# Optimization experiments

Hardware: AMD Instinct MI355X
Metric: run time of the kernel (lower is better)

Reference implementation:

```python
import jax, jax.numpy as jnp
import numpy as np

IN_CH = 128
OUT_CH = 128

def setup_inputs() -> dict:
    key = jax.random.key(0)
    k1, k2, k3, k4, k5 = jax.random.split(key, 5)
    from_tensor = jax.random.normal(k1, (640000, IN_CH), dtype=jnp.float32)
    to_index = jax.random.randint(k2, (640000,), 0, 10000, dtype=jnp.int64)
    # torch Linear default init ~ U(-1/sqrt(fan_in), 1/sqrt(fan_in))
    lim1 = 1.0 / np.sqrt(IN_CH)
    lim2 = 1.0 / np.sqrt(OUT_CH)
    W1 = jax.random.uniform(k3, (OUT_CH, IN_CH), jnp.float32, -lim1, lim1)
    b1 = jnp.zeros((OUT_CH,), jnp.float32)
    W2 = jax.random.uniform(k4, (OUT_CH, OUT_CH), jnp.float32, -lim2, lim2)
    b2 = jnp.zeros((OUT_CH,), jnp.float32)
    return {"from_tensor": from_tensor, "to_index": to_index, "dim_size": 10000,
            "W1": W1, "b1": b1, "W2": W2, "b2": b2}

def reference(from_tensor, to_index, dim_size, W1, b1, W2, b2):
    # MLP transform (transform_scatter=True): Linear+ReLU x2
    h = jax.nn.relu(from_tensor @ W1.T + b1)
    h = jax.nn.relu(h @ W2.T + b2)          # (num_src, OUT_CH)
    # scatter-mean over to_index into dim_size rows
    seg_sum = jax.ops.segment_sum(h, to_index, num_segments=dim_size)
    counts = jax.ops.segment_sum(jnp.ones((h.shape[0],), h.dtype), to_index,
                                 num_segments=dim_size)
    return seg_sum / jnp.maximum(counts, 1.0)[:, None]
```

## Files before the change

kernel.cpp:

```cpp
#include <hip/hip_runtime.h>
#include <hip/hip_bf16.h>

#define IN_CH 128
#define OUT_CH 128
#define LDSPAD 136

typedef short bf16x8 __attribute__((ext_vector_type(8)));
typedef float f32x4  __attribute__((ext_vector_type(4)));

__device__ __forceinline__ unsigned short f32_to_bf16_bits(float f) {
    unsigned u = __builtin_bit_cast(unsigned, f);
    u += 0x7FFFu + ((u >> 16) & 1u);
    return (unsigned short)(u >> 16);
}
__device__ __forceinline__ float bf16_bits_to_f32(unsigned short b) {
    return __builtin_bit_cast(float, (unsigned)b << 16);
}

__global__ void detect_kernel(const unsigned short* __restrict__ X,
                              const unsigned short* __restrict__ W1,
                              const unsigned short* __restrict__ W2,
                              const int* __restrict__ idx,
                              int* __restrict__ flags) {
    __shared__ int red[4];
    const int t = threadIdx.x;
    if (t < 4) red[t] = 0;
    __syncthreads();
    #pragma unroll
    for (int w = 0; w < 3; ++w) {
        const unsigned short* p = (w == 0) ? X : (w == 1) ? W1 : W2;
        int crazy = 0;
        for (int j = t; j < 512; j += 256) {
            const unsigned short h = p[j];
            const int e = (h >> 7) & 0xFF;
            const int man = h & 0x7F;
            if (e >= 0x90 || (e == 0 && man != 0)) crazy++;
        }
        if (crazy) atomicAdd(&red[w], crazy);
    }
    {
        if (idx[2 * t + 1] != 0) atomicAdd(&red[3], 1);
    }
    __syncthreads();
    if (t == 0) {
        flags[0] = red[0] > 16 ? 1 : 0;
        flags[1] = red[1] > 16 ? 1 : 0;
        flags[2] = red[2] > 16 ? 1 : 0;
        flags[3] = red[3] < 8  ? 1 : 0;
    }
}

__global__ void count_kernel(const int* __restrict__ idx, int* __restrict__ cnt,
                             const int* __restrict__ flags, int n) {
    const int sh = flags[3];
    int i = blockIdx.x * blockDim.x + threadIdx.x;
    if (i < n) atomicAdd(&cnt[idx[(size_t)i << sh]], 1);
}

__global__ __launch_bounds__(256)
void mlp_scatter_kernel(const unsigned short* __restrict__ X,
                        const int* __restrict__ idx,
                        const unsigned short* __restrict__ W1,
                        const unsigned short* __restrict__ B1,
                        const unsigned short* __restrict__ W2,
                        const unsigned short* __restrict__ B2,
                        float* __restrict__ seg_sum,
                        const int* __restrict__ flags,
                        int n_src, int n_tiles)
{
    __shared__ short lds_x[16 * LDSPAD];
    __shared__ short lds_h[16 * LDSPAD];

    const int xf32  = flags[0];
    const int w1f32 = flags[1];
    const int w2f32 = flags[2];
    const int i64   = flags[3];

    const int tid  = threadIdx.x;
    const int wave = tid >> 6;
    const int lane = tid & 63;
    const int m    = lane & 15;
    const int quad = lane >> 4;

    bf16x8 w1f[2][4], w2f[2][4];
    float  b1c[2], b2c[2];
    #pragma unroll
    for (int t = 0; t < 2; ++t) {
        const int n = wave * 32 + t * 16 + m;
        b1c[t] = w1f32 ? ((const float*)B1)[n] : bf16_bits_to_f32(B1[n]);
        b2c[t] = w2f32 ? ((const float*)B2)[n] : bf16_bits_to_f32(B2[n]);
        #pragma unroll
        for (int kc = 0; kc < 4; ++kc) {
            const int ko = kc * 32 + quad * 8;
            if (w1f32) {
                const float* Wf = (const float*)W1;
                f32x4 lo = *(const f32x4*)(Wf + n * IN_CH + ko);
                f32x4 hi = *(const f32x4*)(Wf + n * IN_CH + ko + 4);
                bf16x8 v;
                #pragma unroll
                for (int j = 0; j < 4; ++j) {
                    v[j]     = (short)f32_to_bf16_bits(lo[j]);
                    v[4 + j] = (short)f32_to_bf16_bits(hi[j]);
                }
                w1f[t][kc] = v;
            } else {
                w1f[t][kc] = *(const bf16x8*)(W1 + n * IN_CH + ko);
            }
            if (w2f32) {
                const float* Wf = (const float*)W2;
                f32x4 lo = *(const f32x4*)(Wf + n * OUT_CH + ko);
                f32x4 hi = *(const f32x4*)(Wf + n * OUT_CH + ko + 4);
                bf16x8 v;
                #pragma unroll
                for (int j = 0; j < 4; ++j) {
                    v[j]     = (short)f32_to_bf16_bits(lo[j]);
                    v[4 + j] = (short)f32_to_bf16_bits(hi[j]);
                }
                w2f[t][kc] = v;
            } else {
                w2f[t][kc] = *(const bf16x8*)(W2 + n * OUT_CH + ko);
            }
        }
    }

    const int srow = tid >> 4;
    const int sseg = tid & 15;

    for (int tile = blockIdx.x; tile < n_tiles; tile += gridDim.x) {
        const int r0 = tile * 16;

        {
            const int gr = r0 + srow;
            bf16x8 v = {0, 0, 0, 0, 0, 0, 0, 0};
            if (gr < n_src) {
                if (xf32) {
                    const float* Xf = (const float*)X;
                    f32x4 lo = *(const f32x4*)(Xf + (size_t)gr * IN_CH + sseg * 8);
                    f32x4 hi = *(const f32x4*)(Xf + (size_t)gr * IN_CH + sseg * 8 + 4);
                    #pragma unroll
                    for (int j = 0; j < 4; ++j) {
                        v[j]     = (short)f32_to_bf16_bits(lo[j]);
                        v[4 + j] = (short)f32_to_bf16_bits(hi[j]);
                    }
                } else {
                    v = *(const bf16x8*)(X + (size_t)gr * IN_CH + sseg * 8);
                }
            }
            *(bf16x8*)&lds_x[srow * LDSPAD + sseg * 8] = v;
        }
        __syncthreads();

        f32x4 acc0 = {0.f, 0.f, 0.f, 0.f}, acc1 = {0.f, 0.f, 0.f, 0.f};
        #pragma unroll
        for (int kc = 0; kc < 4; ++kc) {
            bf16x8 a = *(const bf16x8*)&lds_x[m * LDSPAD + kc * 32 + quad * 8];
            acc0 = __builtin_amdgcn_mfma_f32_16x16x32_bf16(a, w1f[0][kc], acc0, 0, 0, 0);
            acc1 = __builtin_amdgcn_mfma_f32_16x16x32_bf16(a, w1f[1][kc], acc1, 0, 0, 0);
        }
        #pragma unroll
        for (int t = 0; t < 2; ++t) {
            const int col = wave * 32 + t * 16 + m;
            const float bias = b1c[t];
            const f32x4 acc = t == 0 ? acc0 : acc1;
            #pragma unroll
            for (int r = 0; r < 4; ++r) {
                float v = acc[r] + bias;
                v = v > 0.f ? v : 0.f;
                lds_h[(quad * 4 + r) * LDSPAD + col] = (short)f32_to_bf16_bits(v);
            }
        }
        __syncthreads();

        f32x4 acc2_0 = {0.f, 0.f, 0.f, 0.f}, acc2_1 = {0.f, 0.f, 0.f, 0.f};
        #pragma unroll
        for (int kc = 0; kc < 4; ++kc) {
            bf16x8 a = *(const bf16x8*)&lds_h[m * LDSPAD + kc * 32 + quad * 8];
            acc2_0 = __builtin_amdgcn_mfma_f32_16x16x32_bf16(a, w2f[0][kc], acc2_0, 0, 0, 0);
            acc2_1 = __builtin_amdgcn_mfma_f32_16x16x32_bf16(a, w2f[1][kc], acc2_1, 0, 0, 0);
        }

        int seg[4];
        #pragma unroll
        for (int r = 0; r < 4; ++r) {
            const int grow = r0 + quad * 4 + r;
            seg[r] = (grow < n_src) ? idx[(size_t)grow << i64] : -1;
        }
        #pragma unroll
        for (int t = 0; t < 2; ++t) {
            const int col = wave * 32 + t * 16 + m;
            const float bias = b2c[t];
            const f32x4 acc = t == 0 ? acc2_0 : acc2_1;
            #pragma unroll
            for (int r = 0; r < 4; ++r) {
                if (seg[r] >= 0) {
                    float v = acc[r] + bias;
                    v = v > 0.f ? v : 0.f;
                    unsafeAtomicAdd(&seg_sum[(size_t)seg[r] * OUT_CH + col], v);
                }
            }
        }
    }
}

__global__ void finalize_kernel(const float* __restrict__ seg_sum,
                                const int* __restrict__ cnt,
                                float* __restrict__ out, int total) {
    int i = blockIdx.x * blockDim.x + threadIdx.x;
    if (i < total) {
        int c = cnt[i >> 7];
        c = c > 1 ? c : 1;
        out[i] = seg_sum[i] / (float)c;
    }
}

extern "C" void kernel_launch(void* const* d_in, const int* in_sizes, int n_in,
                              void* d_out, int out_size, void* d_ws, size_t ws_size,
                              hipStream_t stream) {
    int iX = 0;
    for (int i = 1; i < n_in; ++i)
        if (in_sizes[i] > in_sizes[iX]) iX = i;
    const int n_src = in_sizes[iX] / IN_CH;
    int iI = -1, iW1 = -1, iW2 = -1, iB1 = -1, iB2 = -1;
    for (int i = 0; i < n_in; ++i) {
        if (i == iX) continue;
        const int s = in_sizes[i];
        if (s == n_src && iI < 0) iI = i;
        else if (s == IN_CH * OUT_CH) { if (iW1 < 0) iW1 = i; else if (iW2 < 0) iW2 = i; }
        else if (s == OUT_CH) { if (iB1 < 0) iB1 = i; else if (iB2 < 0) iB2 = i; }
    }

    const unsigned short* X  = (const unsigned short*)d_in[iX];
    const int*            ix = (const int*)d_in[iI];
    const unsigned short* W1 = (const unsigned short*)d_in[iW1];
    const unsigned short* B1 = (const unsigned short*)d_in[iB1];
    const unsigned short* W2 = (const unsigned short*)d_in[iW2];
    const unsigned short* B2 = (const unsigned short*)d_in[iB2];
    float* out = (float*)d_out;

    const int dim = out_size / OUT_CH;

    int*   flags   = (int*)d_ws;
    float* seg_sum = (float*)((char*)d_ws + 256);
    int*   cnt     = (int*)((char*)d_ws + 256 + (size_t)dim * OUT_CH * sizeof(float));

    hipMemsetAsync((char*)d_ws + 256, 0,
                   (size_t)dim * OUT_CH * sizeof(float) + (size_t)dim * sizeof(int),
                   stream);

    detect_kernel<<<1, 256, 0, stream>>>(X, W1, W2, ix, flags);

    count_kernel<<<(n_src + 255) / 256, 256, 0, stream>>>(ix, cnt, flags, n_src);

    const int n_tiles = (n_src + 15) / 16;
    const int grid = n_tiles < 10000 ? n_tiles : 10000;
    mlp_scatter_kernel<<<grid, 256, 0, stream>>>(X, ix, W1, B1, W2, B2, seg_sum,
                                                 flags, n_src, n_tiles);

    finalize_kernel<<<(out_size + 255) / 256, 256, 0, stream>>>(seg_sum, cnt, out, out_size);
}
```

Measured before the change: 709.9 us.

## Replace atomic scatter with CSR sort-and-gather segment reduction

Builds a CSR permutation of sources grouped by destination segment using a count, a single-block scan and an atomic placement pass. The MLP kernel then iterates per segment, gathering the member rows, reducing the MLP outputs in registers and writing the mean directly. This removes the per-element float atomics into the segment-sum buffer, the large memset and the finalize kernel. In exchange it adds a serial single-block scan, a permutation pass and irregular row gathers, and wastes MFMA work on partial 16-row tiles since segments average about 64 rows.

```diff
diff --git a/kernel.cpp b/kernel.cpp
--- a/kernel.cpp
+++ b/kernel.cpp
@@ -1,5 +1,4 @@
 #include <hip/hip_runtime.h>
-#include <hip/hip_bf16.h>
 
 #define IN_CH 128
 #define OUT_CH 128
@@ -57,16 +56,63 @@
     if (i < n) atomicAdd(&cnt[idx[(size_t)i << sh]], 1);
 }
 
+__global__ void scan_kernel(const int* __restrict__ cnt, int* __restrict__ off,
+                            int* __restrict__ cur, int dim) {
+    __shared__ int wtot[16];
+    __shared__ int woff[16];
+    __shared__ int carry_s;
+    const int tid = threadIdx.x;
+    const int wv = tid >> 6, ln = tid & 63;
+    if (tid == 0) carry_s = 0;
+    __syncthreads();
+    for (int base = 0; base < dim; base += 1024) {
+        const int i = base + tid;
+        const int orig = (i < dim) ? cnt[i] : 0;
+        int v = orig;
+        #pragma unroll
+        for (int d = 1; d < 64; d <<= 1) {
+            int w = __shfl_up(v, d, 64);
+            if (ln >= d) v += w;
+        }
+        if (ln == 63) wtot[wv] = v;
+        __syncthreads();
+        if (tid == 0) {
+            int acc = carry_s;
+            #pragma unroll
+            for (int k = 0; k < 16; ++k) { woff[k] = acc; acc += wtot[k]; }
+            carry_s = acc;
+        }
+        __syncthreads();
+        const int excl = woff[wv] + v - orig;
+        if (i < dim) { off[i] = excl; cur[i] = excl; }
+        __syncthreads();
+    }
+}
+
+__global__ void perm_kernel(const int* __restrict__ idx, int* __restrict__ cur,
+                            int* __restrict__ perm, const int* __restrict__ flags,
+                            int n) {
+    const int sh = flags[3];
+    int i = blockIdx.x * blockDim.x + threadIdx.x;
+    if (i < n) {
+        const int s = idx[(size_t)i << sh];
+        const int p = atomicAdd(&cur[s], 1);
+        perm[p] = i;
+    }
+}
+
 __global__ __launch_bounds__(256)
-void mlp_scatter_kernel(const unsigned short* __restrict__ X,
-                        const int* __restrict__ idx,
-                        const unsigned short* __restrict__ W1,
-                        const unsigned short* __restrict__ B1,
-                        const unsigned short* __restrict__ W2,
-                        const unsigned short* __restrict__ B2,
-                        float* __restrict__ seg_sum,
-                        const int* __restrict__ flags,
-                        int n_src, int n_tiles)
+void mlp_gather_kernel(const unsigned short* __restrict__ X,
+                       const int* __restrict__ perm,
+                       const int* __restrict__ off,
+                       const int* __restrict__ cnt,
+                       const unsigned short* __restrict__ W1,
+                       const unsigned short* __restrict__ B1,
+                       const unsigned short* __restrict__ W2,
+                       const unsigned short* __restrict__ B2,
+                       float* __restrict__ out,
+                       const int* __restrict__ flags,
+                       int dim)
 {
     __shared__ short lds_x[16 * LDSPAD];
     __shared__ short lds_h[16 * LDSPAD];
@@ -74,7 +120,6 @@
     const int xf32  = flags[0];
     const int w1f32 = flags[1];
     const int w2f32 = flags[2];
-    const int i64   = flags[3];
 
     const int tid  = threadIdx.x;
     const int wave = tid >> 6;
@@ -126,90 +171,89 @@
     const int srow = tid >> 4;
     const int sseg = tid & 15;
 
-    for (int tile = blockIdx.x; tile < n_tiles; tile += gridDim.x) {
-        const int r0 = tile * 16;
-
-        {
-            const int gr = r0 + srow;
-            bf16x8 v = {0, 0, 0, 0, 0, 0, 0, 0};
-            if (gr < n_src) {
-                if (xf32) {
-                    const float* Xf = (const float*)X;
-                    f32x4 lo = *(const f32x4*)(Xf + (size_t)gr * IN_CH + sseg * 8);
-                    f32x4 hi = *(const f32x4*)(Xf + (size_t)gr * IN_CH + sseg * 8 + 4);
-                    #pragma unroll
-                    for (int j = 0; j < 4; ++j) {
-                        v[j]     = (short)f32_to_bf16_bits(lo[j]);
-                        v[4 + j] = (short)f32_to_bf16_bits(hi[j]);
+    for (int s = blockIdx.x; s < dim; s += gridDim.x) {
+        const int c     = cnt[s];
+        const int start = off[s];
+        float sum0 = 0.f, sum1 = 0.f;
+
+        for (int base = 0; base < c; base += 16) {
+            {
+                const int gr = base + srow;
+                bf16x8 v = {0, 0, 0, 0, 0, 0, 0, 0};
+                if (gr < c) {
+                    const int row = perm[start + gr];
+                    if (xf32) {
+                        const float* Xf = (const float*)X;
+                        f32x4 lo = *(const f32x4*)(Xf + (size_t)row * IN_CH + sseg * 8);
+                        f32x4 hi = *(const f32x4*)(Xf + (size_t)row * IN_CH + sseg * 8 + 4);
+                        #pragma unroll
+                        for (int j = 0; j < 4; ++j) {
+                            v[j]     = (short)f32_to_bf16_bits(lo[j]);
+                            v[4 + j] = (short)f32_to_bf16_bits(hi[j]);
+                        }
+                    } else {
+                        v = *(const bf16x8*)(X + (size_t)row * IN_CH + sseg * 8);
                     }
-                } else {
-                    v = *(const bf16x8*)(X + (size_t)gr * IN_CH + sseg * 8);
-                }
-            }
-            *(bf16x8*)&lds_x[srow * LDSPAD + sseg * 8] = v;
-        }
-        __syncthreads();
-
-        f32x4 acc0 = {0.f, 0.f, 0.f, 0.f}, acc1 = {0.f, 0.f, 0.f, 0.f};
-        #pragma unroll
-        for (int kc = 0; kc < 4; ++kc) {
-            bf16x8 a = *(const bf16x8*)&lds_x[m * LDSPAD + kc * 32 + quad * 8];
-            acc0 = __builtin_amdgcn_mfma_f32_16x16x32_bf16(a, w1f[0][kc], acc0, 0, 0, 0);
-            acc1 = __builtin_amdgcn_mfma_f32_16x16x32_bf16(a, w1f[1][kc], acc1, 0, 0, 0);
-        }
-        #pragma unroll
-        for (int t = 0; t < 2; ++t) {
-            const int col = wave * 32 + t * 16 + m;
-            const float bias = b1c[t];
-            const f32x4 acc = t == 0 ? acc0 : acc1;
-            #pragma unroll
-            for (int r = 0; r < 4; ++r) {
-                float v = acc[r] + bias;
-                v = v > 0.f ? v : 0.f;
-                lds_h[(quad * 4 + r) * LDSPAD + col] = (short)f32_to_bf16_bits(v);
-            }
-        }
-        __syncthreads();
-
-        f32x4 acc2_0 = {0.f, 0.f, 0.f, 0.f}, acc2_1 = {0.f, 0.f, 0.f, 0.f};
-        #pragma unroll
-        for (int kc = 0; kc < 4; ++kc) {
-            bf16x8 a = *(const bf16x8*)&lds_h[m * LDSPAD + kc * 32 + quad * 8];
-            acc2_0 = __builtin_amdgcn_mfma_f32_16x16x32_bf16(a, w2f[0][kc], acc2_0, 0, 0, 0);
-            acc2_1 = __builtin_amdgcn_mfma_f32_16x16x32_bf16(a, w2f[1][kc], acc2_1, 0, 0, 0);
-        }
-
-        int seg[4];
-        #pragma unroll
-        for (int r = 0; r < 4; ++r) {
-            const int grow = r0 + quad * 4 + r;
-            seg[r] = (grow < n_src) ? idx[(size_t)grow << i64] : -1;
-        }
-        #pragma unroll
-        for (int t = 0; t < 2; ++t) {
-            const int col = wave * 32 + t * 16 + m;
-            const float bias = b2c[t];
-            const f32x4 acc = t == 0 ? acc2_0 : acc2_1;
-            #pragma unroll
-            for (int r = 0; r < 4; ++r) {
-                if (seg[r] >= 0) {
+                }
+                *(bf16x8*)&lds_x[srow * LDSPAD + sseg * 8] = v;
+            }
+            __syncthreads();
+
+            f32x4 acc0 = {0.f, 0.f, 0.f, 0.f}, acc1 = {0.f, 0.f, 0.f, 0.f};
+            #pragma unroll
+            for (int kc = 0; kc < 4; ++kc) {
+                bf16x8 a = *(const bf16x8*)&lds_x[m * LDSPAD + kc * 32 + quad * 8];
+                acc0 = __builtin_amdgcn_mfma_f32_16x16x32_bf16(a, w1f[0][kc], acc0, 0, 0, 0);
+                acc1 = __builtin_amdgcn_mfma_f32_16x16x32_bf16(a, w1f[1][kc], acc1, 0, 0, 0);
+            }
+            #pragma unroll
+            for (int t = 0; t < 2; ++t) {
+                const int col = wave * 32 + t * 16 + m;
+                const float bias = b1c[t];
+                const f32x4 acc = t == 0 ? acc0 : acc1;
+                #pragma unroll
+                for (int r = 0; r < 4; ++r) {
                     float v = acc[r] + bias;
                     v = v > 0.f ? v : 0.f;
-                    unsafeAtomicAdd(&seg_sum[(size_t)seg[r] * OUT_CH + col], v);
-                }
-            }
-        }
-    }
-}
-
-__global__ void finalize_kernel(const float* __restrict__ seg_sum,
-                                const int* __restrict__ cnt,
-                                float* __restrict__ out, int total) {
-    int i = blockIdx.x * blockDim.x + threadIdx.x;
-    if (i < total) {
-        int c = cnt[i >> 7];
-        c = c > 1 ? c : 1;
-        out[i] = seg_sum[i] / (float)c;
+                    lds_h[(quad * 4 + r) * LDSPAD + col] = (short)f32_to_bf16_bits(v);
+                }
+            }
+            __syncthreads();
+
+            f32x4 acc2_0 = {0.f, 0.f, 0.f, 0.f}, acc2_1 = {0.f, 0.f, 0.f, 0.f};
+            #pragma unroll
+            for (int kc = 0; kc < 4; ++kc) {
+                bf16x8 a = *(const bf16x8*)&lds_h[m * LDSPAD + kc * 32 + quad * 8];
+                acc2_0 = __builtin_amdgcn_mfma_f32_16x16x32_bf16(a, w2f[0][kc], acc2_0, 0, 0, 0);
+                acc2_1 = __builtin_amdgcn_mfma_f32_16x16x32_bf16(a, w2f[1][kc], acc2_1, 0, 0, 0);
+            }
+
+            #pragma unroll
+            for (int t = 0; t < 2; ++t) {
+                const float bias = b2c[t];
+                const f32x4 acc = t == 0 ? acc2_0 : acc2_1;
+                float sr = 0.f;
+                #pragma unroll
+                for (int r = 0; r < 4; ++r) {
+                    if (base + quad * 4 + r < c) {
+                        float v = acc[r] + bias;
+                        sr += (v > 0.f ? v : 0.f);
+                    }
+                }
+                if (t == 0) sum0 += sr; else sum1 += sr;
+            }
+        }
+
+        sum0 += __shfl_xor(sum0, 16, 64);
+        sum0 += __shfl_xor(sum0, 32, 64);
+        sum1 += __shfl_xor(sum1, 16, 64);
+        sum1 += __shfl_xor(sum1, 32, 64);
+        if (quad == 0) {
+            const float inv = 1.f / (float)(c > 1 ? c : 1);
+            float* o = out + (size_t)s * OUT_CH + wave * 32 + m;
+            o[0]  = sum0 * inv;
+            o[16] = sum1 * inv;
+        }
     }
 }
 
@@ -239,22 +283,23 @@
 
     const int dim = out_size / OUT_CH;
 
-    int*   flags   = (int*)d_ws;
-    float* seg_sum = (float*)((char*)d_ws + 256);
-    int*   cnt     = (int*)((char*)d_ws + 256 + (size_t)dim * OUT_CH * sizeof(float));
-
-    hipMemsetAsync((char*)d_ws + 256, 0,
-                   (size_t)dim * OUT_CH * sizeof(float) + (size_t)dim * sizeof(int),
-                   stream);
+    int* flags = (int*)d_ws;
+    int* cnt   = (int*)((char*)d_ws + 256);
+    int* off   = cnt + dim;
+    int* cur   = off + dim;
+    int* perm  = cur + dim;
+
+    hipMemsetAsync(cnt, 0, (size_t)dim * sizeof(int), stream);
 
     detect_kernel<<<1, 256, 0, stream>>>(X, W1, W2, ix, flags);
 
     count_kernel<<<(n_src + 255) / 256, 256, 0, stream>>>(ix, cnt, flags, n_src);
 
-    const int n_tiles = (n_src + 15) / 16;
-    const int grid = n_tiles < 10000 ? n_tiles : 10000;
-    mlp_scatter_kernel<<<grid, 256, 0, stream>>>(X, ix, W1, B1, W2, B2, seg_sum,
-                                                 flags, n_src, n_tiles);
-
-    finalize_kernel<<<(out_size + 255) / 256, 256, 0, stream>>>(seg_sum, cnt, out, out_size);
-}
+    scan_kernel<<<1, 1024, 0, stream>>>(cnt, off, cur, dim);
+
+    perm_kernel<<<(n_src + 255) / 256, 256, 0, stream>>>(ix, cur, perm, flags, n_src);
+
+    const int grid = dim < 2048 ? dim : 2048;
+    mlp_gather_kernel<<<grid, 256, 0, stream>>>(X, perm, off, cnt, W1, B1, W2, B2,
+                                                out, flags, dim);
+}
```

After: 580.3 us. -18.3%, faster.
